# Optimization experiments

Measured on AMD Instinct MI355X. Metric: run time of the kernel, lower is better.

## Reference

```python
import jax, jax.numpy as jnp
import numpy as np

B, N, T, F, H, DK, DV, DM, K, C = 16, 1024, 12, 1, 3, 32, 32, 512, 3, 64


def _ln(x, g, b, eps=1e-5):
    mu = x.mean(-1, keepdims=True)
    var = ((x - mu) ** 2).mean(-1, keepdims=True)
    return (x - mu) / jnp.sqrt(var + eps) * g + b


def setup_inputs() -> dict:
    ks = jax.random.split(jax.random.key(0), 32)
    it = iter(range(32))
    def nrm(shape, s=0.02):
        return jax.random.normal(ks[next(it)], shape, jnp.float32) * s
    d = {
        'x': jax.random.normal(ks[next(it)], (B, N, F, T), jnp.float32),
        'res_att': jnp.zeros((B, F, H, T, T), jnp.float32),
        'pos_T': nrm((T, N)), 'gT': jnp.ones(N), 'bT': jnp.zeros(N),
        'wq': nrm((N, H * DK)), 'wk': nrm((N, H * DK)), 'wv': nrm((N, H * DV)),
        'fc': nrm((H * DV, N)),
        'pre_w': nrm((DM, T, F)), 'pre_b': jnp.zeros(DM),
        'pos_S': nrm((N, DM)), 'gS': jnp.ones(DM), 'bS': jnp.zeros(DM),
        'swq': nrm((DM, K * DK)), 'swk': nrm((DM, K * DK)),
        'cheb': nrm((K, N, N), 0.1),
        'adj_pa': jax.random.uniform(ks[next(it)], (N, N), jnp.float32),
        'cmask': nrm((K, N, N)),
        'theta': nrm((K, F, C)),
        'g3w': nrm((2 * C, C, 1, 3)), 'g3b': jnp.zeros(2 * C),
        'g5w': nrm((2 * C, C, 1, 5)), 'g5b': jnp.zeros(2 * C),
        'g7w': nrm((2 * C, C, 1, 7)), 'g7b': jnp.zeros(2 * C),
        'fcw': nrm((3 * T - 12, T)), 'fcb': jnp.zeros(T),
        'rw': nrm((C, F)), 'rb': jnp.zeros(C),
        'gln': jnp.ones(C), 'bln': jnp.zeros(C),
    }
    return d


def reference(x, res_att, pos_T, gT, bT, wq, wk, wv, fc, pre_w, pre_b,
              pos_S, gS, bS, swq, swk, cheb, adj_pa, cmask, theta,
              g3w, g3b, g5w, g5b, g7w, g7b, fcw, fcb, rw, rb, gln, bln):
    Bsz, Nv, Fin, Ts = x.shape
    # --- EmbedT (num_of_features == 1 path): x (B,N,F,T) -> (B,F,T,N) + pos emb, LN over N
    TEmx = _ln(jnp.transpose(x, (0, 2, 3, 1)) + pos_T[None, None], gT, bT)
    # --- temporal multi-head attention over T (d_model == N)
    def heads(z, w, d):  # (B,F,T,N)@(N,H*d) -> (B,F,H,T,d)
        return jnp.transpose(jnp.einsum('bftn,nk->bftk', z, w).reshape(Bsz, Fin, Ts, H, d), (0, 1, 3, 2, 4))
    Q = heads(TEmx, wq, DK)
    Kh = heads(TEmx, wk, DK)
    V = heads(TEmx, wv, DV)
    scores = jnp.einsum('bfhqd,bfhkd->bfhqk', Q, Kh) / np.float32(np.sqrt(DK)) + res_att
    attn = jax.nn.softmax(scores, axis=3)  # NOTE: dim=3 as in original code (query axis)
    ctx = jnp.einsum('bfhqk,bfhkd->bfhqd', attn, V)
    ctx = jnp.transpose(ctx, (0, 1, 3, 2, 4)).reshape(Bsz, Fin, Ts, H * DV)
    one = jnp.ones((Nv,), x.dtype); zero = jnp.zeros((Nv,), x.dtype)
    TATout = _ln(ctx @ fc + TEmx, one, zero)  # fresh LayerNorm(d_model) -> no learned affine
    # --- pre_conv: Conv2d(T, d_model, kernel (1,F)) on (B,T,N,F), take [...,-1] -> (B,N,d_model)
    x_TAt = jnp.einsum('bftn,dtf->bnd', TATout, pre_w) + pre_b
    # --- EmbedS + spatial attention scores (no softmax), n_heads = K
    SEmx = _ln(x_TAt + pos_S[None], gS, bS)
    SQ = jnp.transpose((SEmx @ swq).reshape(Bsz, Nv, K, DK), (0, 2, 1, 3))
    SK = jnp.transpose((SEmx @ swk).reshape(Bsz, Nv, K, DK), (0, 2, 1, 3))
    STAt = jnp.einsum('bknd,bkmd->bknm', SQ, SK) / np.float32(np.sqrt(DK))  # (B,K,N,N)
    # --- Chebyshev graph conv with spatial attention (vectorized over k and t)
    satt = jax.nn.softmax(STAt + (adj_pa[None] * cmask)[None], axis=2)  # softmax over rows (dim=1 of NxN)
    A = cheb[None] * satt  # (B,K,N,N)
    rhs = jnp.einsum('bknm,bnft->bkmft', A, x)  # T_k_with_at^T @ graph_signal for all t
    spatial_gcn = jax.nn.relu(jnp.einsum('bkmft,kfo->bmot', rhs, theta))  # (B,N,C,T)
    X = jnp.transpose(spatial_gcn, (0, 2, 1, 3))  # (B,C,N,T)
    # --- parallel GTU gated temporal convs
    def gtu(z, w, b):
        y = jax.lax.conv_general_dilated(z, w, (1, 1), 'VALID',
                                         dimension_numbers=('NCHW', 'OIHW', 'NCHW')) + b[None, :, None, None]
        return jnp.tanh(y[:, :C]) * jax.nn.sigmoid(y[:, C:])
    tc = jnp.concatenate([gtu(X, g3w, g3b), gtu(X, g5w, g5b), gtu(X, g7w, g7b)], axis=-1)  # (B,C,N,3T-12)
    time_conv = tc @ fcw + fcb  # fcmy Linear(3T-12 -> T); dropout is identity in eval
    time_conv_output = jax.nn.relu(time_conv)  # num_of_features == 1 branch
    # --- residual 1x1 conv (num_of_features == 1 branch)
    x_residual = jnp.einsum('bfnt,cf->bcnt', jnp.transpose(x, (0, 2, 1, 3)), rw) + rb[None, :, None, None]
    out = jax.nn.relu(x_residual + time_conv_output)  # (B,C,N,T)
    out = _ln(jnp.transpose(out, (0, 3, 2, 1)), gln, bln)  # LN over nb_time_filter
    out = jnp.transpose(out, (0, 2, 3, 1))  # (B,N,C,T)
    return out, scores
```

## Files before the change

### kernel.cpp

```cpp
#include <hip/hip_runtime.h>
#include <hip/hip_fp16.h>

#define EPS 1e-5f

typedef float f32x4 __attribute__((ext_vector_type(4)));
typedef short bf16x8 __attribute__((ext_vector_type(8)));
typedef short bf16x4 __attribute__((ext_vector_type(4)));

__device__ __forceinline__ unsigned short f2b(float f){
  unsigned u=__float_as_uint(f);
  return (unsigned short)((u + 0x7fffu + ((u>>16)&1u))>>16);
}
__device__ __forceinline__ float b2f(unsigned short h){
  return __uint_as_float(((unsigned)h)<<16);
}

__device__ __forceinline__ float blockSum256(float v, float* red){
  #pragma unroll
  for(int o=32;o>0;o>>=1) v += __shfl_down(v,o,64);
  int wid = threadIdx.x>>6;
  if((threadIdx.x&63)==0) red[wid]=v;
  __syncthreads();
  if(threadIdx.x==0) red[0]=red[0]+red[1]+red[2]+red[3];
  __syncthreads();
  float r = red[0];
  __syncthreads();
  return r;
}

__global__ __launch_bounds__(256) void kbp_prep(const float* __restrict__ adj, const float* __restrict__ cmask,
    const float* __restrict__ cheb, unsigned* __restrict__ mcT,
    const float* __restrict__ g3w, const float* __restrict__ g5w,
    const float* __restrict__ g7w, const float* __restrict__ swq, const float* __restrict__ swk,
    const float* __restrict__ wq, const float* __restrict__ wk, const float* __restrict__ wv,
    const float* __restrict__ fcw, const float* __restrict__ fcW,
    unsigned short* __restrict__ Apack, unsigned short* __restrict__ Wpack,
    unsigned short* __restrict__ Wpack2, unsigned short* __restrict__ fcwB,
    unsigned short* __restrict__ fcWB2){
  int tid=threadIdx.x;
  if(blockIdx.x<768){
    int blk=blockIdx.x;
    int k=blk>>8; int rem=blk&255; int tn=rem>>4, tm=rem&15;
    __shared__ unsigned tile[64][65];
    const float* chk = cheb + k*1048576;
    const float* cmk = cmask + k*1048576;
    for(int i=tid;i<4096;i+=256){
      int ln=i>>6, lm=i&63;
      int n=tn*64+ln, m=tm*64+lm;
      int nm=n*1024+m;
      tile[ln][lm] = (((unsigned)f2b(chk[nm]))<<16) | (unsigned)f2b(adj[nm]*cmk[nm]);
    }
    __syncthreads();
    unsigned* dst = mcT + k*1048576;
    for(int i=tid;i<4096;i+=256){
      int lm=i>>6, ln=i&63;
      dst[(tm*64+lm)*1024 + tn*64+ln] = tile[ln][lm];
    }
    return;
  }
  int idx = (blockIdx.x-768)*256+tid;
  if(idx<15360){
    int frag=idx>>6, lane=idx&63;
    int rt, s, kappa; const float* W;
    if(frag<48){ rt=frag/6; s=frag-rt*6; kappa=3; W=g3w; }
    else if(frag<128){ int f=frag-48; rt=f/10; s=f-rt*10; kappa=5; W=g5w; }
    else { int f=frag-128; rt=f/14; s=f-rt*14; kappa=7; W=g7w; }
    int c = rt*16 + (lane&15);
    int dt = s>>1, ic0=(s&1)*32 + (lane>>4)*8;
    #pragma unroll
    for(int j=0;j<8;j++) Apack[idx*8+j]=f2b(W[(c*64+ic0+j)*kappa + dt]);
  } else if(idx<27648){
    int id2=idx-15360;
    int frag=id2>>6, lane=id2&63;
    int ct=frag>>4, ks=frag&15;
    const float* W = (ct<6)? swq : swk;
    int c = ((ct<6)? ct : ct-6)*16 + (lane&15);
    int k0 = ks*32 + (lane>>4)*8;
    #pragma unroll
    for(int j=0;j<8;j++) Wpack[id2*8+j]=f2b(W[(k0+j)*96 + c]);
  } else if(idx<64512){
    int id2=idx-27648;
    int frag=id2>>6, lane=id2&63;
    int ct=frag>>5, ks=frag&31;
    int cg = ct*16 + (lane&15);
    const float* W; int c;
    if(cg<96){ W=wq; c=cg; } else if(cg<192){ W=wk; c=cg-96; } else { W=wv; c=cg-192; }
    int k0 = ks*32 + (lane>>4)*8;
    #pragma unroll
    for(int j=0;j<8;j++) Wpack2[id2*8+j]=f2b(W[(k0+j)*96 + c]);
  } else if(idx<64576){
    int lane=idx-64512;
    int t=lane&15, hq=lane>>4;
    #pragma unroll
    for(int j=0;j<8;j++){
      int tau=hq*8+j;
      fcwB[lane*8+j] = (tau<24 && t<12) ? f2b(fcw[tau*12+t]) : (unsigned short)0;
    }
  } else if(idx<76864){
    int id3=idx-64576;
    int frag=id3>>6, lane=id3&63;
    int ct=frag/3, ks=frag-ct*3;
    int c = ct*16 + (lane&15);
    int k0 = ks*32 + (lane>>4)*8;
    #pragma unroll
    for(int j=0;j<8;j++) fcWB2[id3*8+j]=f2b(fcW[(k0+j)*1024 + c]);
  }
}

__global__ __launch_bounds__(256) void k1_embedT(const float* __restrict__ x, const float* __restrict__ posT,
    const float* __restrict__ gT, const float* __restrict__ bT, float* __restrict__ TEmx,
    unsigned short* __restrict__ TEb){
  int bt=blockIdx.x; int b=bt/12, t=bt-b*12;
  int tid=threadIdx.x;
  __shared__ float red[4];
  float v[4]; float s=0.f;
  #pragma unroll
  for(int i=0;i<4;i++){ int n=tid+i*256; v[i]=x[(b*1024+n)*12+t]+posT[t*1024+n]; s+=v[i]; }
  s = blockSum256(s, red);
  float mu = s*(1.f/1024.f);
  float q=0.f;
  #pragma unroll
  for(int i=0;i<4;i++){ float d=v[i]-mu; q+=d*d; }
  q = blockSum256(q, red);
  float rstd = rsqrtf(q*(1.f/1024.f)+EPS);
  #pragma unroll
  for(int i=0;i<4;i++){
    int n=tid+i*256;
    float val=(v[i]-mu)*rstd*gT[n]+bT[n];
    TEmx[bt*1024+n]=val;
    TEb[bt*1024+n]=f2b(val);
  }
}

__global__ __launch_bounds__(256) void k2_qkv(const unsigned short* __restrict__ TEb,
    const unsigned short* __restrict__ Wpack2, float* __restrict__ qkv){
  int tid=threadIdx.x; int w=tid>>6, lane=tid&63;
  const int hi=lane>>4, lo=lane&15;
  const int rt=blockIdx.x/18, ct=blockIdx.x-rt*18;
  __shared__ float red[4][16][16];
  f32x4 acc={0.f,0.f,0.f,0.f};
  #pragma unroll
  for(int s=0;s<8;s++){
    int ks=w*8+s;
    bf16x8 af = *(const bf16x8*)&TEb[(rt*16+lo)*1024 + ks*32 + hi*8];
    bf16x8 bf = *(const bf16x8*)&Wpack2[((ct*32+ks)<<9) + lane*8];
    acc = __builtin_amdgcn_mfma_f32_16x16x32_bf16(af, bf, acc, 0,0,0);
  }
  #pragma unroll
  for(int r=0;r<4;r++) red[w][hi*4+r][lo]=acc[r];
  __syncthreads();
  int r16=tid>>4, c16=tid&15;
  float s = red[0][r16][c16]+red[1][r16][c16]+red[2][r16][c16]+red[3][r16][c16];
  qkv[(rt*16+r16)*288 + ct*16 + c16] = s;
}

__global__ __launch_bounds__(256) void k3_attn(const float* __restrict__ qkv, const float* __restrict__ res_att,
    float* __restrict__ scores_out, unsigned short* __restrict__ ctxb){
  int bh=blockIdx.x; int b=bh/3, h=bh-(bh/3)*3;
  int tid=threadIdx.x;
  __shared__ float sS[144];
  __shared__ float sA[144];
  if(tid<144){
    int q=tid/12;
    const float* Qr=&qkv[(b*12+q)*288 + h*32];
    const float* Kr=&qkv[(b*12+(tid-q*12))*288 + 96 + h*32];
    float acc=0.f;
    #pragma unroll
    for(int d=0;d<32;d++) acc+=Qr[d]*Kr[d];
    acc = acc*0.17677669529663687f + res_att[bh*144 + tid];
    sS[tid]=acc;
    scores_out[bh*144 + tid]=acc;
  }
  __syncthreads();
  if(tid<12){
    int k2=tid;
    float mx=-1e30f;
    for(int q=0;q<12;q++) mx=fmaxf(mx,sS[q*12+k2]);
    float sum=0.f;
    for(int q=0;q<12;q++){ float e=__expf(sS[q*12+k2]-mx); sA[q*12+k2]=e; sum+=e; }
    float inv=1.f/sum;
    for(int q=0;q<12;q++) sA[q*12+k2]*=inv;
  }
  __syncthreads();
  for(int o=tid;o<384;o+=256){
    int q=o>>5, d=o&31;
    float acc=0.f;
    #pragma unroll
    for(int k2=0;k2<12;k2++) acc += sA[q*12+k2]*qkv[(b*12+k2)*288+192+h*32+d];
    ctxb[(b*12+q)*96 + h*32 + d]=f2b(acc);
  }
}

__global__ __launch_bounds__(256) void k4a_mm(const unsigned short* __restrict__ ctxb,
    const unsigned short* __restrict__ fcWB2, const float* __restrict__ TEmx,
    float* __restrict__ TATpre){
  int tid=threadIdx.x; int w=tid>>6, lane=tid&63;
  const int hi=lane>>4, lo=lane&15;
  const int rt=blockIdx.x>>4, cg=blockIdx.x&15;
  const int ct=cg*4+w;
  f32x4 acc={0.f,0.f,0.f,0.f};
  #pragma unroll
  for(int ks=0;ks<3;ks++){
    bf16x8 af = *(const bf16x8*)&ctxb[(rt*16+lo)*96 + ks*32 + hi*8];
    bf16x8 bf = *(const bf16x8*)&fcWB2[((ct*3+ks)<<9) + lane*8];
    acc = __builtin_amdgcn_mfma_f32_16x16x32_bf16(af, bf, acc, 0,0,0);
  }
  #pragma unroll
  for(int r=0;r<4;r++){
    int row = rt*16 + hi*4 + r;
    int coln = ct*16 + lo;
    TATpre[row*1024+coln] = acc[r] + TEmx[row*1024+coln];
  }
}

__global__ __launch_bounds__(256) void k4b_stats(const float* __restrict__ TATpre,
    float* __restrict__ muT, float* __restrict__ rsT){
  int bt=blockIdx.x; int tid=threadIdx.x;
  __shared__ float red[4];
  const float* row=&TATpre[bt*1024];
  float a0=row[tid], a1=row[tid+256], a2=row[tid+512], a3=row[tid+768];
  float s=a0+a1+a2+a3;
  s=blockSum256(s,red);
  float mu=s*(1.f/1024.f);
  float q=(a0-mu)*(a0-mu)+(a1-mu)*(a1-mu)+(a2-mu)*(a2-mu)+(a3-mu)*(a3-mu);
  q=blockSum256(q,red);
  if(tid==0){ muT[bt]=mu; rsT[bt]=rsqrtf(q*(1.f/1024.f)+EPS); }
}

__global__ __launch_bounds__(256) void k5_semx(const float* __restrict__ TATpre,
    const float* __restrict__ muT, const float* __restrict__ rsT,
    const float* __restrict__ pre_w,
    const float* __restrict__ pre_b, const float* __restrict__ posS, const float* __restrict__ gS,
    const float* __restrict__ bS, unsigned short* __restrict__ SEb){
  int bn0=blockIdx.x*8; int b=bn0>>10, n0=bn0&1023; int tid=threadIdx.x;
  __shared__ float tv[12][8];
  __shared__ float ps[8][264];
  __shared__ float pq[8][264];
  __shared__ float mur[8], rsr[8];
  if(tid<96){
    int r=tid&7, t=tid>>3;
    int bt=b*12+t;
    tv[t][r]=(TATpre[bt*1024+n0+r]-muT[bt])*rsT[bt];
  }
  __syncthreads();
  const int d0=tid, d1=tid+256;
  float w0[12], w1[12];
  {
    const float4* p0=(const float4*)&pre_w[d0*12];
    float4 a=p0[0], bb=p0[1], c=p0[2];
    w0[0]=a.x;w0[1]=a.y;w0[2]=a.z;w0[3]=a.w; w0[4]=bb.x;w0[5]=bb.y;w0[6]=bb.z;w0[7]=bb.w;
    w0[8]=c.x;w0[9]=c.y;w0[10]=c.z;w0[11]=c.w;
    const float4* p1=(const float4*)&pre_w[d1*12];
    float4 d=p1[0], e=p1[1], f=p1[2];
    w1[0]=d.x;w1[1]=d.y;w1[2]=d.z;w1[3]=d.w; w1[4]=e.x;w1[5]=e.y;w1[6]=e.z;w1[7]=e.w;
    w1[8]=f.x;w1[9]=f.y;w1[10]=f.z;w1[11]=f.w;
  }
  float pb0=pre_b[d0], pb1=pre_b[d1];
  float v0[8], v1[8];
  #pragma unroll
  for(int r=0;r<8;r++){
    float acc0=pb0 + posS[(n0+r)*512+d0];
    float acc1=pb1 + posS[(n0+r)*512+d1];
    #pragma unroll
    for(int t=0;t<12;t++){ float tvv=tv[t][r]; acc0+=tvv*w0[t]; acc1+=tvv*w1[t]; }
    v0[r]=acc0; v1[r]=acc1;
    ps[r][tid]=acc0+acc1;
    pq[r][tid]=acc0*acc0+acc1*acc1;
  }
  __syncthreads();
  {
    int row=tid>>5, l32=tid&31;
    float s=0.f, q=0.f;
    #pragma unroll
    for(int j=0;j<8;j++){ s+=ps[row][l32+j*32]; q+=pq[row][l32+j*32]; }
    #pragma unroll
    for(int o=16;o>=1;o>>=1){ s+=__shfl_xor(s,o,64); q+=__shfl_xor(q,o,64); }
    if(l32==0){
      float mu=s*(1.f/512.f);
      float var=q*(1.f/512.f)-mu*mu;
      mur[row]=mu; rsr[row]=rsqrtf(var+EPS);
    }
  }
  __syncthreads();
  float g0=gS[d0], b0v=bS[d0], g1=gS[d1], b1v=bS[d1];
  #pragma unroll
  for(int r=0;r<8;r++){
    float mu=mur[r], rs=rsr[r];
    SEb[(bn0+r)*512 + d0] = f2b((v0[r]-mu)*rs*g0+b0v);
    SEb[(bn0+r)*512 + d1] = f2b((v1[r]-mu)*rs*g1+b1v);
  }
}

__global__ __launch_bounds__(256) void k6_sqk(const unsigned short* __restrict__ SEb,
    const unsigned short* __restrict__ Wpack,
    unsigned short* __restrict__ SQb, unsigned short* __restrict__ SKb){
  int tid=threadIdx.x; int w=tid>>6, lane=tid&63;
  const int hi=lane>>4, lo=lane&15;
  const int row0 = blockIdx.x*16;
  f32x4 acc[3];
  #pragma unroll
  for(int i=0;i<3;i++){ acc[i][0]=0.f; acc[i][1]=0.f; acc[i][2]=0.f; acc[i][3]=0.f; }
  const unsigned short* arow = &SEb[(row0+lo)*512 + hi*8];
  bf16x8 afc = *(const bf16x8*)&arow[0];
  #pragma unroll
  for(int ks=0;ks<16;ks++){
    bf16x8 afn;
    if(ks<15) afn = *(const bf16x8*)&arow[(ks+1)*32];
    #pragma unroll
    for(int j=0;j<3;j++){
      int ct = w*3+j;
      bf16x8 bf = *(const bf16x8*)&Wpack[((ct*16+ks)<<9) + lane*8];
      acc[j] = __builtin_amdgcn_mfma_f32_16x16x32_bf16(afc, bf, acc[j], 0,0,0);
    }
    if(ks<15) afc = afn;
  }
  #pragma unroll
  for(int j=0;j<3;j++){
    int ct = w*3+j;
    int c96 = ((ct<6)? ct : ct-6)*16 + lo;
    int kq = c96>>5, d = c96&31;
    unsigned short* dst = (ct<6)? SQb : SKb;
    #pragma unroll
    for(int r=0;r<4;r++){
      int n = row0 + hi*4 + r;
      int b = n>>10, nl = n&1023;
      dst[((b*3+kq)*1024+nl)*32 + d] = f2b(acc[j][r]);
    }
  }
}

#define SCALE7 0.17677669529663687f
__global__ __launch_bounds__(256) void k7_spatial(const unsigned short* __restrict__ SQb,
    const unsigned short* __restrict__ SKb, const unsigned* __restrict__ mcT,
    const float* __restrict__ x, float* __restrict__ rhsT){
  const int blk0=blockIdx.x;
  const int blk=(blk0&7)*96 + (blk0>>3);
  const int mt=blk&15, bk=blk>>4;
  const int k=bk%3, b=bk/3;
  const int m0=mt*64;
  const int tid=threadIdx.x;
  const int w=tid>>6, lane=tid&63, g=lane>>4, col=lane&15;

  __shared__ unsigned short xs[16*1024];

  const float* xb = x + b*12288;
  for(int i=tid;i<2048;i+=256) ((unsigned*)xs)[12*512 + i] = 0u;
  for(int i=tid;i<12288;i+=256){
    int n=i/12, t=i-n*12;
    xs[t*1024 + (n ^ ((t&7)<<3))] = f2b(xb[i]);
  }
  __syncthreads();

  const int m_glob = m0 + w*16 + col;
  bf16x8 bfrag = *(const bf16x8*)&SKb[((bk<<10)+m_glob)*32 + g*8];

  f32x4 O = {0.f,0.f,0.f,0.f};
  float mrun=-1e30f, lrun=0.f;

  const unsigned* mrow = mcT + k*1048576 + m_glob*1024;
  const unsigned short* sqbase = &SQb[((bk<<10)+col)*32 + g*8];
  const int swz = (col&7)<<3;

  uint4 mvc[8]; bf16x8 afc[8];
  #pragma unroll
  for(int nt=0;nt<8;nt++){
    mvc[nt] = *(const uint4*)&mrow[nt*16 + g*4];
    afc[nt] = *(const bf16x8*)&sqbase[(nt*16)*32];
  }

  #pragma unroll
  for(int ch=0; ch<8; ++ch){
    const int n0 = ch<<7;
    uint4 mvn[8]; bf16x8 afn[8];
    #pragma unroll
    for(int nt=0;nt<8;nt++){
      if(ch<7){
        mvn[nt] = *(const uint4*)&mrow[n0+128 + nt*16 + g*4];
        afn[nt] = *(const bf16x8*)&sqbase[(n0+128 + nt*16)*32];
      }
    }

    f32x4 acc[8];
    #pragma unroll
    for(int nt=0;nt<8;nt++){
      f32x4 z = {0.f,0.f,0.f,0.f};
      acc[nt] = __builtin_amdgcn_mfma_f32_16x16x32_bf16(afc[nt], bfrag, z, 0,0,0);
    }
    float cmax = -1e30f;
    #pragma unroll
    for(int nt=0;nt<8;nt++){
      #pragma unroll
      for(int r=0;r<4;r++){
        unsigned mv = (r==0)?mvc[nt].x:((r==1)?mvc[nt].y:((r==2)?mvc[nt].z:mvc[nt].w));
        float s = acc[nt][r]*SCALE7 + __uint_as_float(mv<<16);
        acc[nt][r]=s;
        cmax=fmaxf(cmax,s);
      }
    }
    cmax = fmaxf(cmax, __shfl_xor(cmax,16,64));
    cmax = fmaxf(cmax, __shfl_xor(cmax,32,64));
    float mnew = fmaxf(mrun, cmax);
    float alpha = __expf(mrun - mnew);
    float lsum = 0.f;
    unsigned short pb[8][4];
    #pragma unroll
    for(int nt=0;nt<8;nt++){
      #pragma unroll
      for(int r=0;r<4;r++){
        unsigned mv = (r==0)?mvc[nt].x:((r==1)?mvc[nt].y:((r==2)?mvc[nt].z:mvc[nt].w));
        float e = __expf(acc[nt][r] - mnew);
        lsum += e;
        pb[nt][r] = f2b(e * __uint_as_float(mv & 0xffff0000u));
      }
    }
    lsum += __shfl_xor(lsum,16,64);
    lsum += __shfl_xor(lsum,32,64);
    lrun = lrun*alpha + lsum;
    mrun = mnew;
    O[0]*=alpha; O[1]*=alpha; O[2]*=alpha; O[3]*=alpha;

    #pragma unroll
    for(int c=0;c<4;c++){
      bf16x8 pf;
      #pragma unroll
      for(int j=0;j<4;j++){ pf[j]=(short)pb[2*c][j]; pf[j+4]=(short)pb[2*c+1][j]; }
      int nlo = n0 + c*32 + g*4;
      bf16x4 lo = *(const bf16x4*)&xs[col*1024 + (nlo ^ swz)];
      bf16x4 hi = *(const bf16x4*)&xs[col*1024 + ((nlo+16) ^ swz)];
      bf16x8 ax;
      #pragma unroll
      for(int j=0;j<4;j++){ ax[j]=lo[j]; ax[j+4]=hi[j]; }
      O = __builtin_amdgcn_mfma_f32_16x16x32_bf16(ax, pf, O, 0,0,0);
    }
    #pragma unroll
    for(int nt=0;nt<8;nt++){
      if(ch<7){ mvc[nt]=mvn[nt]; afc[nt]=afn[nt]; }
    }
  }
  float inv = 1.f/lrun;
  #pragma unroll
  for(int r=0;r<4;r++){
    int t = g*4+r;
    if(t<12) rhsT[((bk*12+t)<<10) + m_glob] = O[r]*inv;
  }
}

__global__ __launch_bounds__(256) void k9_final(const float* __restrict__ rhsT, const float* __restrict__ theta,
    const unsigned short* __restrict__ Apack, const unsigned short* __restrict__ fcwB,
    const float* __restrict__ g3b, const float* __restrict__ g5b, const float* __restrict__ g7b,
    const float* __restrict__ fcb,
    const float* __restrict__ rw, const float* __restrict__ rb,
    const float* __restrict__ gln, const float* __restrict__ bln,
    const float* __restrict__ x, float* __restrict__ out){
  int bn0=blockIdx.x*8;
  int tid=threadIdx.x;
  const int b=bn0>>10, n0=bn0&1023;

  __shared__ struct { unsigned short Xl[12*8*64]; float rstage[3][12][8]; } P0;
  __shared__ union {
    unsigned short Gl[4*16*8*24];
    float XP[8][772];
  } U;
  __shared__ float xres[8][12];
  __shared__ float mu8[8][12], rs8[8][12];

  for(int i=tid;i<288;i+=256){
    int kk=i/96; int rem=i-kk*96; int t=rem>>3; int g=rem&7;
    P0.rstage[kk][t][g]=rhsT[((b*3+kk)*12+t)*1024 + n0 + g];
  }
  for(int i=tid;i<96;i+=256){ int g=i/12, t=i-(i/12)*12; xres[g][t]=x[(bn0+g)*12+t]; }
  __syncthreads();

  {
    int g=tid>>5, icp=tid&31;
    float th0[3], th1[3];
    #pragma unroll
    for(int kk=0;kk<3;kk++){ th0[kk]=theta[kk*64+2*icp]; th1[kk]=theta[kk*64+2*icp+1]; }
    #pragma unroll
    for(int t=0;t<12;t++){
      float r0=P0.rstage[0][t][g], r1=P0.rstage[1][t][g], r2=P0.rstage[2][t][g];
      float a0=fmaxf(r0*th0[0]+r1*th0[1]+r2*th0[2],0.f);
      float a1=fmaxf(r0*th1[0]+r1*th1[1]+r2*th1[2],0.f);
      unsigned pack = (((unsigned)f2b(a1))<<16)|(unsigned)f2b(a0);
      *(unsigned*)((char*)P0.Xl + ((t*8+g)<<7) + ((icp*4) ^ (g<<4))) = pack;
    }
  }
  __syncthreads();

  const int w=tid>>6, lane=tid&63, halfk=lane>>4, colq=lane&15;
  const int gg=colq&7, tau2=colq>>3;
  const int ca = w*16 + halfk*4;
  const char* xlb = (const char*)P0.Xl;
  unsigned short* Glw = &U.Gl[w*3072];

  #define GATE_STORE(ACCA, ACCB, TB) { \
    _Pragma("unroll") \
    for(int r=0;r<4;r++){ \
      float ya=(ACCA)[r], yb=(ACCB)[r]; \
      float e2=__expf(2.f*ya), eb=__expf(yb); \
      float gval=(e2-1.f)*eb*__frcp_rn((e2+1.f)*(eb+1.f)); \
      int c_loc=halfk*4+r; \
      Glw[c_loc*192 + ((gg ^ (c_loc&7))*24) + (TB)+tau2] = f2b(gval); \
    } }

  {
    f32x4 acA[5], acB[5];
    #pragma unroll
    for(int j=0;j<5;j++)
      #pragma unroll
      for(int r=0;r<4;r++){ acA[j][r]=g3b[ca+r]; acB[j][r]=g3b[64+ca+r]; }
    const unsigned short* ap0=&Apack[((w  )*6)*512 + lane*8];
    const unsigned short* ap1=&Apack[((w+4)*6)*512 + lane*8];
    bf16x8 a0c=*(const bf16x8*)&ap0[0];
    bf16x8 a1c=*(const bf16x8*)&ap1[0];
    #pragma unroll
    for(int s=0;s<6;s++){
      bf16x8 a0n, a1n;
      if(s<5){ a0n=*(const bf16x8*)&ap0[(s+1)*512]; a1n=*(const bf16x8*)&ap1[(s+1)*512]; }
      int dt=s>>1;
      int sl = ((((s&1)*32 + halfk*8)*2) ^ (gg<<4));
      __builtin_amdgcn_s_setprio(1);
      #pragma unroll
      for(int j=0;j<5;j++){
        int t=2*j+tau2+dt;
        bf16x8 bf = *(const bf16x8*)(xlb + ((t*8+gg)<<7) + sl);
        acA[j] = __builtin_amdgcn_mfma_f32_16x16x32_bf16(a0c, bf, acA[j], 0,0,0);
        acB[j] = __builtin_amdgcn_mfma_f32_16x16x32_bf16(a1c, bf, acB[j], 0,0,0);
      }
      __builtin_amdgcn_s_setprio(0);
      if(s<5){ a0c=a0n; a1c=a1n; }
    }
    #pragma unroll
    for(int j=0;j<5;j++) GATE_STORE(acA[j], acB[j], 2*j)
  }
  {
    f32x4 acA[4], acB[4];
    #pragma unroll
    for(int j=0;j<4;j++)
      #pragma unroll
      for(int r=0;r<4;r++){ acA[j][r]=g5b[ca+r]; acB[j][r]=g5b[64+ca+r]; }
    const unsigned short* ap0=&Apack[(48 + (w  )*10)*512 + lane*8];
    const unsigned short* ap1=&Apack[(48 + (w+4)*10)*512 + lane*8];
    bf16x8 a0c=*(const bf16x8*)&ap0[0];
    bf16x8 a1c=*(const bf16x8*)&ap1[0];
    #pragma unroll
    for(int s=0;s<10;s++){
      bf16x8 a0n, a1n;
      if(s<9){ a0n=*(const bf16x8*)&ap0[(s+1)*512]; a1n=*(const bf16x8*)&ap1[(s+1)*512]; }
      int dt=s>>1;
      int sl = ((((s&1)*32 + halfk*8)*2) ^ (gg<<4));
      __builtin_amdgcn_s_setprio(1);
      #pragma unroll
      for(int j=0;j<4;j++){
        int t=2*j+tau2+dt;
        bf16x8 bf = *(const bf16x8*)(xlb + ((t*8+gg)<<7) + sl);
        acA[j] = __builtin_amdgcn_mfma_f32_16x16x32_bf16(a0c, bf, acA[j], 0,0,0);
        acB[j] = __builtin_amdgcn_mfma_f32_16x16x32_bf16(a1c, bf, acB[j], 0,0,0);
      }
      __builtin_amdgcn_s_setprio(0);
      if(s<9){ a0c=a0n; a1c=a1n; }
    }
    #pragma unroll
    for(int j=0;j<4;j++) GATE_STORE(acA[j], acB[j], 10+2*j)
  }
  {
    f32x4 acA[3], acB[3];
    #pragma unroll
    for(int j=0;j<3;j++)
      #pragma unroll
      for(int r=0;r<4;r++){ acA[j][r]=g7b[ca+r]; acB[j][r]=g7b[64+ca+r]; }
    const unsigned short* ap0=&Apack[(128 + (w  )*14)*512 + lane*8];
    const unsigned short* ap1=&Apack[(128 + (w+4)*14)*512 + lane*8];
    bf16x8 a0c=*(const bf16x8*)&ap0[0];
    bf16x8 a1c=*(const bf16x8*)&ap1[0];
    #pragma unroll
    for(int s=0;s<14;s++){
      bf16x8 a0n, a1n;
      if(s<13){ a0n=*(const bf16x8*)&ap0[(s+1)*512]; a1n=*(const bf16x8*)&ap1[(s+1)*512]; }
      int dt=s>>1;
      int sl = ((((s&1)*32 + halfk*8)*2) ^ (gg<<4));
      __builtin_amdgcn_s_setprio(1);
      #pragma unroll
      for(int j=0;j<3;j++){
        int t=2*j+tau2+dt;
        bf16x8 bf = *(const bf16x8*)(xlb + ((t*8+gg)<<7) + sl);
        acA[j] = __builtin_amdgcn_mfma_f32_16x16x32_bf16(a0c, bf, acA[j], 0,0,0);
        acB[j] = __builtin_amdgcn_mfma_f32_16x16x32_bf16(a1c, bf, acB[j], 0,0,0);
      }
      __builtin_amdgcn_s_setprio(0);
      if(s<13){ a0c=a0n; a1c=a1n; }
    }
    #pragma unroll
    for(int j=0;j<3;j++) GATE_STORE(acA[j], acB[j], 18+2*j)
  }
  #undef GATE_STORE

  const int tcol = lane&15, hq = lane>>4;
  const int hm = (hq==3)? 0 : hq;
  bf16x8 b2 = *(const bf16x8*)&fcwB[lane*8];
  float fcbv = (tcol<12)? fcb[tcol] : 0.f;
  f32x4 d2[8];
  #pragma unroll
  for(int g=0; g<8; g++){
    bf16x8 a2 = *(const bf16x8*)&Glw[tcol*192 + ((g ^ (tcol&7))*24) + hm*8];
    f32x4 ini = {fcbv, fcbv, fcbv, fcbv};
    d2[g] = __builtin_amdgcn_mfma_f32_16x16x32_bf16(a2, b2, ini, 0,0,0);
  }
  __syncthreads();

  if(tcol<12){
    float rwa[4], rba[4];
    #pragma unroll
    for(int r=0;r<4;r++){ int c=w*16+hq*4+r; rwa[r]=rw[c]; rba[r]=rb[c]; }
    #pragma unroll
    for(int g=0; g<8; g++){
      float xv=xres[g][tcol];
      #pragma unroll
      for(int r=0;r<4;r++){
        int c=w*16+hq*4+r;
        float tv = fmaxf(d2[g][r], 0.f);
        float xr = xv*rwa[r]+rba[r];
        U.XP[g][c*12+tcol] = fmaxf(xr+tv, 0.f);
      }
    }
  }
  __syncthreads();

  if(tid<192){
    int p=tid>>1, h=tid&1;
    int g=p/12, t=p-(p/12)*12;
    float s=0.f;
    for(int c=h*32;c<h*32+32;c++) s+=U.XP[g][c*12+t];
    s += __shfl_xor(s,1,64);
    float mu=s*(1.f/64.f);
    float q=0.f;
    for(int c=h*32;c<h*32+32;c++){float d=U.XP[g][c*12+t]-mu;q+=d*d;}
    q += __shfl_xor(q,1,64);
    if(h==0){ mu8[g][t]=mu; rs8[g][t]=rsqrtf(q*(1.f/64.f)+EPS); }
  }
  __syncthreads();
  for(int o=tid;o<1536;o+=256){
    int g=o/192; int q4=o-g*192;
    int c=q4/3; int tb=(q4-c*3)*4;
    float4 vv = *(const float4*)&U.XP[g][c*12+tb];
    float gl=gln[c], bl=bln[c];
    float4 ov;
    ov.x=(vv.x-mu8[g][tb+0])*rs8[g][tb+0]*gl+bl;
    ov.y=(vv.y-mu8[g][tb+1])*rs8[g][tb+1]*gl+bl;
    ov.z=(vv.z-mu8[g][tb+2])*rs8[g][tb+2]*gl+bl;
    ov.w=(vv.w-mu8[g][tb+3])*rs8[g][tb+3]*gl+bl;
    *(float4*)&out[(long)(bn0+g)*768 + c*12 + tb] = ov;
  }
}

extern "C" void kernel_launch(void* const* d_in, const int* in_sizes, int n_in,
                              void* d_out, int out_size, void* d_ws, size_t ws_size,
                              hipStream_t stream){
  const float* x    =(const float*)d_in[0];
  const float* res  =(const float*)d_in[1];
  const float* posT =(const float*)d_in[2];
  const float* gT   =(const float*)d_in[3];
  const float* bT   =(const float*)d_in[4];
  const float* wq   =(const float*)d_in[5];
  const float* wk   =(const float*)d_in[6];
  const float* wv   =(const float*)d_in[7];
  const float* fcW  =(const float*)d_in[8];
  const float* prw  =(const float*)d_in[9];
  const float* prb  =(const float*)d_in[10];
  const float* posS =(const float*)d_in[11];
  const float* gS   =(const float*)d_in[12];
  const float* bS   =(const float*)d_in[13];
  const float* swq  =(const float*)d_in[14];
  const float* swk  =(const float*)d_in[15];
  const float* cheb =(const float*)d_in[16];
  const float* adj  =(const float*)d_in[17];
  const float* cmask=(const float*)d_in[18];
  const float* theta=(const float*)d_in[19];
  const float* g3w=(const float*)d_in[20]; const float* g3b=(const float*)d_in[21];
  const float* g5w=(const float*)d_in[22]; const float* g5b=(const float*)d_in[23];
  const float* g7w=(const float*)d_in[24]; const float* g7b=(const float*)d_in[25];
  const float* fcw=(const float*)d_in[26]; const float* fcb=(const float*)d_in[27];
  const float* rw =(const float*)d_in[28]; const float* rb =(const float*)d_in[29];
  const float* gln=(const float*)d_in[30]; const float* bln=(const float*)d_in[31];

  float* outp=(float*)d_out;
  float* scores = outp + 12582912;

  float* wsf=(float*)d_ws;
  float* TEmx = wsf;
  float* qkv  = TEmx + 196608;
  float* TATpre = qkv + 55296;
  unsigned short* SEb = (unsigned short*)(TATpre + 196608);
  unsigned short* SQb = (unsigned short*)((float*)SEb + 4194304);
  unsigned short* SKb = (unsigned short*)((float*)SQb + 786432);
  unsigned* mcT = (unsigned*)((float*)SKb + 786432);
  float* rhsT  = (float*)mcT + 3145728;
  unsigned short* Apack = (unsigned short*)(rhsT + 589824);
  unsigned short* Wpack = Apack + 122880;
  unsigned short* Wpack2 = Wpack + 98304;
  unsigned short* TEb = Wpack2 + 294912;
  unsigned short* fcwB = TEb + 196608;
  unsigned short* ctxb = fcwB + 512;
  unsigned short* fcWB2 = ctxb + 18432;
  float* muT = (float*)(fcWB2 + 98304);
  float* rsT = muT + 192;

  kbp_prep<<<dim3(1069),dim3(256),0,stream>>>(adj,cmask,cheb,mcT,
                                              g3w,g5w,g7w,swq,swk,wq,wk,wv,fcw,fcW,
                                              Apack,Wpack,Wpack2,fcwB,fcWB2);
  k1_embedT<<<dim3(192),dim3(256),0,stream>>>(x,posT,gT,bT,TEmx,TEb);
  k2_qkv<<<dim3(216),dim3(256),0,stream>>>(TEb,Wpack2,qkv);
  k3_attn<<<dim3(48),dim3(256),0,stream>>>(qkv,res,scores,ctxb);
  k4a_mm<<<dim3(192),dim3(256),0,stream>>>(ctxb,fcWB2,TEmx,TATpre);
  k4b_stats<<<dim3(192),dim3(256),0,stream>>>(TATpre,muT,rsT);
  k5_semx<<<dim3(2048),dim3(256),0,stream>>>(TATpre,muT,rsT,prw,prb,posS,gS,bS,SEb);
  k6_sqk<<<dim3(1024),dim3(256),0,stream>>>(SEb,Wpack,SQb,SKb);
  k7_spatial<<<dim3(768),dim3(256),0,stream>>>(SQb,SKb,mcT,x,rhsT);
  k9_final<<<dim3(2048),dim3(256),0,stream>>>(rhsT,theta,Apack,fcwB,g3b,g5b,g7b,
                                              fcb,rw,rb,gln,bln,x,outp);
}
```

Before: 141.3 us.

## Fuse embedT into prep kernel and spatial embedding LN into SQ/SK matmul

The temporal embedding/LayerNorm blocks are appended to the weight-prep kernel's grid, removing one launch. The spatial embedding LayerNorm now writes its bf16 rows into shared memory and the same block runs the SQ/SK MFMA projection, so the SEb intermediate never goes through global memory and another launch is removed. Each fused block handles 16 rows in two passes of 8, which adds extra syncs and about 16KB of LDS per block and may lower occupancy.

```diff
diff --git a/kernel.cpp b/kernel.cpp
--- a/kernel.cpp
+++ b/kernel.cpp
@@ -28,7 +28,7 @@
   return r;
 }
 
-__global__ __launch_bounds__(256) void kbp_prep(const float* __restrict__ adj, const float* __restrict__ cmask,
+__global__ __launch_bounds__(256) void kbp1_prep(const float* __restrict__ adj, const float* __restrict__ cmask,
     const float* __restrict__ cheb, unsigned* __restrict__ mcT,
     const float* __restrict__ g3w, const float* __restrict__ g5w,
     const float* __restrict__ g7w, const float* __restrict__ swq, const float* __restrict__ swk,
@@ -36,25 +36,49 @@
     const float* __restrict__ fcw, const float* __restrict__ fcW,
     unsigned short* __restrict__ Apack, unsigned short* __restrict__ Wpack,
     unsigned short* __restrict__ Wpack2, unsigned short* __restrict__ fcwB,
-    unsigned short* __restrict__ fcWB2){
+    unsigned short* __restrict__ fcWB2,
+    const float* __restrict__ x, const float* __restrict__ posT,
+    const float* __restrict__ gT, const float* __restrict__ bT,
+    float* __restrict__ TEmx, unsigned short* __restrict__ TEb){
   int tid=threadIdx.x;
+  __shared__ union { unsigned tile[64][65]; float red[4]; } SH;
   if(blockIdx.x<768){
     int blk=blockIdx.x;
     int k=blk>>8; int rem=blk&255; int tn=rem>>4, tm=rem&15;
-    __shared__ unsigned tile[64][65];
     const float* chk = cheb + k*1048576;
     const float* cmk = cmask + k*1048576;
     for(int i=tid;i<4096;i+=256){
       int ln=i>>6, lm=i&63;
       int n=tn*64+ln, m=tm*64+lm;
       int nm=n*1024+m;
-      tile[ln][lm] = (((unsigned)f2b(chk[nm]))<<16) | (unsigned)f2b(adj[nm]*cmk[nm]);
+      SH.tile[ln][lm] = (((unsigned)f2b(chk[nm]))<<16) | (unsigned)f2b(adj[nm]*cmk[nm]);
     }
     __syncthreads();
     unsigned* dst = mcT + k*1048576;
     for(int i=tid;i<4096;i+=256){
       int lm=i>>6, ln=i&63;
-      dst[(tm*64+lm)*1024 + tn*64+ln] = tile[ln][lm];
+      dst[(tm*64+lm)*1024 + tn*64+ln] = SH.tile[ln][lm];
+    }
+    return;
+  }
+  if(blockIdx.x>=1069){
+    int bt=blockIdx.x-1069; int b=bt/12, t=bt-b*12;
+    float v[4]; float s=0.f;
+    #pragma unroll
+    for(int i=0;i<4;i++){ int n=tid+i*256; v[i]=x[(b*1024+n)*12+t]+posT[t*1024+n]; s+=v[i]; }
+    s = blockSum256(s, SH.red);
+    float mu = s*(1.f/1024.f);
+    float q=0.f;
+    #pragma unroll
+    for(int i=0;i<4;i++){ float d=v[i]-mu; q+=d*d; }
+    q = blockSum256(q, SH.red);
+    float rstd = rsqrtf(q*(1.f/1024.f)+EPS);
+    #pragma unroll
+    for(int i=0;i<4;i++){
+      int n=tid+i*256;
+      float val=(v[i]-mu)*rstd*gT[n]+bT[n];
+      TEmx[bt*1024+n]=val;
+      TEb[bt*1024+n]=f2b(val);
     }
     return;
   }
@@ -104,31 +128,6 @@
     int k0 = ks*32 + (lane>>4)*8;
     #pragma unroll
     for(int j=0;j<8;j++) fcWB2[id3*8+j]=f2b(fcW[(k0+j)*1024 + c]);
-  }
-}
-
-__global__ __launch_bounds__(256) void k1_embedT(const float* __restrict__ x, const float* __restrict__ posT,
-    const float* __restrict__ gT, const float* __restrict__ bT, float* __restrict__ TEmx,
-    unsigned short* __restrict__ TEb){
-  int bt=blockIdx.x; int b=bt/12, t=bt-b*12;
-  int tid=threadIdx.x;
-  __shared__ float red[4];
-  float v[4]; float s=0.f;
-  #pragma unroll
-  for(int i=0;i<4;i++){ int n=tid+i*256; v[i]=x[(b*1024+n)*12+t]+posT[t*1024+n]; s+=v[i]; }
-  s = blockSum256(s, red);
-  float mu = s*(1.f/1024.f);
-  float q=0.f;
-  #pragma unroll
-  for(int i=0;i<4;i++){ float d=v[i]-mu; q+=d*d; }
-  q = blockSum256(q, red);
-  float rstd = rsqrtf(q*(1.f/1024.f)+EPS);
-  #pragma unroll
-  for(int i=0;i<4;i++){
-    int n=tid+i*256;
-    float val=(v[i]-mu)*rstd*gT[n]+bT[n];
-    TEmx[bt*1024+n]=val;
-    TEb[bt*1024+n]=f2b(val);
   }
 }
 
@@ -227,18 +226,20 @@
   if(tid==0){ muT[bt]=mu; rsT[bt]=rsqrtf(q*(1.f/1024.f)+EPS); }
 }
 
-__global__ __launch_bounds__(256) void k5_semx(const float* __restrict__ TATpre,
+__global__ __launch_bounds__(256) void k56_semx_sqk(const float* __restrict__ TATpre,
     const float* __restrict__ muT, const float* __restrict__ rsT,
-    const float* __restrict__ pre_w,
-    const float* __restrict__ pre_b, const float* __restrict__ posS, const float* __restrict__ gS,
-    const float* __restrict__ bS, unsigned short* __restrict__ SEb){
-  int bn0=blockIdx.x*8; int b=bn0>>10, n0=bn0&1023; int tid=threadIdx.x;
-  __shared__ float tv[12][8];
+    const float* __restrict__ pre_w, const float* __restrict__ pre_b,
+    const float* __restrict__ posS, const float* __restrict__ gS, const float* __restrict__ bS,
+    const unsigned short* __restrict__ Wpack,
+    unsigned short* __restrict__ SQb, unsigned short* __restrict__ SKb){
+  int bn0=blockIdx.x*16; int b=bn0>>10, n0=bn0&1023; int tid=threadIdx.x;
+  __shared__ unsigned short SEl[16*520];
+  __shared__ float tv[12][16];
   __shared__ float ps[8][264];
   __shared__ float pq[8][264];
   __shared__ float mur[8], rsr[8];
-  if(tid<96){
-    int r=tid&7, t=tid>>3;
+  if(tid<192){
+    int r=tid&15, t=tid>>4;
     int bt=b*12+t;
     tv[t][r]=(TATpre[bt*1024+n0+r]-muT[bt])*rsT[bt];
   }
@@ -256,63 +257,59 @@
     w1[8]=f.x;w1[9]=f.y;w1[10]=f.z;w1[11]=f.w;
   }
   float pb0=pre_b[d0], pb1=pre_b[d1];
-  float v0[8], v1[8];
-  #pragma unroll
-  for(int r=0;r<8;r++){
-    float acc0=pb0 + posS[(n0+r)*512+d0];
-    float acc1=pb1 + posS[(n0+r)*512+d1];
-    #pragma unroll
-    for(int t=0;t<12;t++){ float tvv=tv[t][r]; acc0+=tvv*w0[t]; acc1+=tvv*w1[t]; }
-    v0[r]=acc0; v1[r]=acc1;
-    ps[r][tid]=acc0+acc1;
-    pq[r][tid]=acc0*acc0+acc1*acc1;
-  }
-  __syncthreads();
-  {
-    int row=tid>>5, l32=tid&31;
-    float s=0.f, q=0.f;
-    #pragma unroll
-    for(int j=0;j<8;j++){ s+=ps[row][l32+j*32]; q+=pq[row][l32+j*32]; }
-    #pragma unroll
-    for(int o=16;o>=1;o>>=1){ s+=__shfl_xor(s,o,64); q+=__shfl_xor(q,o,64); }
-    if(l32==0){
-      float mu=s*(1.f/512.f);
-      float var=q*(1.f/512.f)-mu*mu;
-      mur[row]=mu; rsr[row]=rsqrtf(var+EPS);
-    }
-  }
-  __syncthreads();
   float g0=gS[d0], b0v=bS[d0], g1=gS[d1], b1v=bS[d1];
-  #pragma unroll
-  for(int r=0;r<8;r++){
-    float mu=mur[r], rs=rsr[r];
-    SEb[(bn0+r)*512 + d0] = f2b((v0[r]-mu)*rs*g0+b0v);
-    SEb[(bn0+r)*512 + d1] = f2b((v1[r]-mu)*rs*g1+b1v);
-  }
-}
-
-__global__ __launch_bounds__(256) void k6_sqk(const unsigned short* __restrict__ SEb,
-    const unsigned short* __restrict__ Wpack,
-    unsigned short* __restrict__ SQb, unsigned short* __restrict__ SKb){
-  int tid=threadIdx.x; int w=tid>>6, lane=tid&63;
+  for(int rb=0;rb<2;rb++){
+    const int rbase=rb*8;
+    float v0[8], v1[8];
+    #pragma unroll
+    for(int r=0;r<8;r++){
+      int rr=rbase+r;
+      float acc0=pb0 + posS[(n0+rr)*512+d0];
+      float acc1=pb1 + posS[(n0+rr)*512+d1];
+      #pragma unroll
+      for(int t=0;t<12;t++){ float tvv=tv[t][rr]; acc0+=tvv*w0[t]; acc1+=tvv*w1[t]; }
+      v0[r]=acc0; v1[r]=acc1;
+      ps[r][tid]=acc0+acc1;
+      pq[r][tid]=acc0*acc0+acc1*acc1;
+    }
+    __syncthreads();
+    {
+      int row=tid>>5, l32=tid&31;
+      float s=0.f, q=0.f;
+      #pragma unroll
+      for(int j=0;j<8;j++){ s+=ps[row][l32+j*32]; q+=pq[row][l32+j*32]; }
+      #pragma unroll
+      for(int o=16;o>=1;o>>=1){ s+=__shfl_xor(s,o,64); q+=__shfl_xor(q,o,64); }
+      if(l32==0){
+        float mu=s*(1.f/512.f);
+        float var=q*(1.f/512.f)-mu*mu;
+        mur[row]=mu; rsr[row]=rsqrtf(var+EPS);
+      }
+    }
+    __syncthreads();
+    #pragma unroll
+    for(int r=0;r<8;r++){
+      float mu=mur[r], rs=rsr[r];
+      SEl[(rbase+r)*520 + d0] = f2b((v0[r]-mu)*rs*g0+b0v);
+      SEl[(rbase+r)*520 + d1] = f2b((v1[r]-mu)*rs*g1+b1v);
+    }
+    __syncthreads();
+  }
+  int w=tid>>6, lane=tid&63;
   const int hi=lane>>4, lo=lane&15;
-  const int row0 = blockIdx.x*16;
   f32x4 acc[3];
   #pragma unroll
   for(int i=0;i<3;i++){ acc[i][0]=0.f; acc[i][1]=0.f; acc[i][2]=0.f; acc[i][3]=0.f; }
-  const unsigned short* arow = &SEb[(row0+lo)*512 + hi*8];
-  bf16x8 afc = *(const bf16x8*)&arow[0];
+  const unsigned short* arow = &SEl[lo*520 + hi*8];
   #pragma unroll
   for(int ks=0;ks<16;ks++){
-    bf16x8 afn;
-    if(ks<15) afn = *(const bf16x8*)&arow[(ks+1)*32];
+    bf16x8 af = *(const bf16x8*)&arow[ks*32];
     #pragma unroll
     for(int j=0;j<3;j++){
       int ct = w*3+j;
       bf16x8 bf = *(const bf16x8*)&Wpack[((ct*16+ks)<<9) + lane*8];
-      acc[j] = __builtin_amdgcn_mfma_f32_16x16x32_bf16(afc, bf, acc[j], 0,0,0);
-    }
-    if(ks<15) afc = afn;
+      acc[j] = __builtin_amdgcn_mfma_f32_16x16x32_bf16(af, bf, acc[j], 0,0,0);
+    }
   }
   #pragma unroll
   for(int j=0;j<3;j++){
@@ -322,9 +319,9 @@
     unsigned short* dst = (ct<6)? SQb : SKb;
     #pragma unroll
     for(int r=0;r<4;r++){
-      int n = row0 + hi*4 + r;
-      int b = n>>10, nl = n&1023;
-      dst[((b*3+kq)*1024+nl)*32 + d] = f2b(acc[j][r]);
+      int n = bn0 + hi*4 + r;
+      int bb2 = n>>10, nl = n&1023;
+      dst[((bb2*3+kq)*1024+nl)*32 + d] = f2b(acc[j][r]);
     }
   }
 }
@@ -705,16 +702,16 @@
   float* muT = (float*)(fcWB2 + 98304);
   float* rsT = muT + 192;
 
-  kbp_prep<<<dim3(1069),dim3(256),0,stream>>>(adj,cmask,cheb,mcT,
-                                              g3w,g5w,g7w,swq,swk,wq,wk,wv,fcw,fcW,
-                                              Apack,Wpack,Wpack2,fcwB,fcWB2);
-  k1_embedT<<<dim3(192),dim3(256),0,stream>>>(x,posT,gT,bT,TEmx,TEb);
+  kbp1_prep<<<dim3(1261),dim3(256),0,stream>>>(adj,cmask,cheb,mcT,
+                                               g3w,g5w,g7w,swq,swk,wq,wk,wv,fcw,fcW,
+                                               Apack,Wpack,Wpack2,fcwB,fcWB2,
+                                               x,posT,gT,bT,TEmx,TEb);
   k2_qkv<<<dim3(216),dim3(256),0,stream>>>(TEb,Wpack2,qkv);
   k3_attn<<<dim3(48),dim3(256),0,stream>>>(qkv,res,scores,ctxb);
   k4a_mm<<<dim3(192),dim3(256),0,stream>>>(ctxb,fcWB2,TEmx,TATpre);
   k4b_stats<<<dim3(192),dim3(256),0,stream>>>(TATpre,muT,rsT);
-  k5_semx<<<dim3(2048),dim3(256),0,stream>>>(TATpre,muT,rsT,prw,prb,posS,gS,bS,SEb);
-  k6_sqk<<<dim3(1024),dim3(256),0,stream>>>(SEb,Wpack,SQb,SKb);
+  k56_semx_sqk<<<dim3(1024),dim3(256),0,stream>>>(TATpre,muT,rsT,prw,prb,posS,gS,bS,
+                                                  Wpack,SQb,SKb);
   k7_spatial<<<dim3(768),dim3(256),0,stream>>>(SQb,SKb,mcT,x,rhsT);
   k9_final<<<dim3(2048),dim3(256),0,stream>>>(rhsT,theta,Apack,fcwB,g3b,g5b,g7b,
                                               fcb,rw,rb,gln,bln,x,outp);
```

Result: faster. 131.0 us (-7.2%).
